# Kernel tuning notes

Hardware: AMD Instinct MI355X
Metric: run time of the kernel (lower is better)

## Reference

```python
import jax, jax.numpy as jnp
import numpy as np

GROUP = 32  # hadamard_group_size == MXFP4 block size
FP4_GRID = np.array([0.0, 0.5, 1.0, 1.5, 2.0, 3.0, 4.0, 6.0], dtype=np.float32)  # e2m1 magnitudes
FP4_MID = np.array([0.25, 0.75, 1.25, 1.75, 2.5, 3.5, 5.0], dtype=np.float32)    # RTN midpoints


def _hadamard(n):
    # Sylvester construction, normalized so H is orthonormal (matches hadamard(n)*n**-0.5)
    H = np.array([[1.0]], dtype=np.float64)
    while H.shape[0] < n:
        H = np.block([[H, H], [H, -H]])
    return (H / np.sqrt(n)).astype(np.float32)


def _pseudo_quant_mxfp4(t, H, gs):
    """Hadamard-rotate per group of 32, then MXFP4 (e2m1 + power-of-two block scale)
    quant-dequant with abs_max scaling and a global scale. STE through the rounding."""
    shp = t.shape
    rot = t.reshape(-1, GROUP) @ H                      # [n_groups, 32] rotated space
    v = jax.lax.stop_gradient(rot) * gs
    absmax = jnp.max(jnp.abs(v), axis=-1, keepdims=True)
    # E8M0 power-of-two shared scale so that absmax/scale <= 6 (max e2m1 value)
    scale = jnp.exp2(jnp.ceil(jnp.log2(absmax / 6.0 + 1e-30)))
    scale = jnp.where(absmax > 0, scale, 1.0)
    u = v / scale
    grid = jnp.asarray(FP4_GRID)
    mid = jnp.asarray(FP4_MID)
    q = jnp.sign(u) * grid[jnp.searchsorted(mid, jnp.abs(u))]  # round-to-nearest e2m1
    dq = q * scale / gs
    out = rot + jax.lax.stop_gradient(dq - rot)         # straight-through estimator
    return out.reshape(shp)


def setup_inputs() -> dict:
    key = jax.random.key(0)
    kx, kw, kb = jax.random.split(key, 3)
    B, S, K, N = 4, 2048, 4096, 4096
    x = jax.random.normal(kx, (B, S, K), jnp.float32)
    weight = jax.random.normal(kw, (N, K), jnp.float32) * (K ** -0.5)
    bias = jax.random.normal(kb, (N,), jnp.float32)
    H = jnp.asarray(_hadamard(GROUP))
    weight_global_scale = jnp.array([3.0], jnp.float32)  # abs_max method
    act_global_scale = jnp.array([3.0], jnp.float32)
    return {"x": x, "weight": weight, "bias": bias, "hadamard_matrix": H,
            "weight_global_scale": weight_global_scale, "act_global_scale": act_global_scale}


def reference(x, weight, bias, hadamard_matrix, weight_global_scale, act_global_scale):
    x_dq = _pseudo_quant_mxfp4(x, hadamard_matrix, act_global_scale[0])
    w_dq = _pseudo_quant_mxfp4(weight, hadamard_matrix, weight_global_scale[0])
    # both operands stay in the rotated space; per-group Hadamard is orthogonal so
    # x_rot @ w_rot^T == x @ w^T up to quantization error (QuTLASS semantics)
    return jnp.einsum('bsk,nk->bsn', x_dq, w_dq) + bias
```

## Files before the change

### kernel.cpp

```cpp
#include <hip/hip_runtime.h>
#include <hip/hip_bf16.h>

typedef int   i32x4  __attribute__((ext_vector_type(4)));
typedef int   i32x8  __attribute__((ext_vector_type(8)));
typedef float f32x16 __attribute__((ext_vector_type(16)));

__device__ inline void gload_lds16(const void* g, void* l) {
  __builtin_amdgcn_global_load_lds((const __attribute__((address_space(1))) void*)g,
                                   (__attribute__((address_space(3))) void*)l, 16, 0, 0);
}
__device__ inline void gload_lds4(const void* g, void* l) {
  __builtin_amdgcn_global_load_lds((const __attribute__((address_space(1))) void*)g,
                                   (__attribute__((address_space(3))) void*)l, 4, 0, 0);
}

__global__ __launch_bounds__(256) void quant_fused(const float* __restrict__ x,
                                                   const float* __restrict__ wt,
                                                   unsigned char* __restrict__ xq,
                                                   unsigned char* __restrict__ xsc,
                                                   unsigned char* __restrict__ wq,
                                                   unsigned char* __restrict__ wsc,
                                                   const float* __restrict__ ags,
                                                   const float* __restrict__ wgs,
                                                   int xg, int Mrows, int Nrows, int kg) {
  const int first = blockIdx.x * 256;
  const bool isX = first < xg;
  const float* in        = isX ? x   : wt;
  unsigned char* outq    = isX ? xq  : wq;
  unsigned char* outsc   = isX ? xsc : wsc;
  const float gs         = isX ? ags[0] : wgs[0];
  const int rows         = isX ? Mrows : Nrows;
  const int base         = isX ? first : first - xg;
  const int g = base + threadIdx.x;
  const int r = g / kg, j = g - r * kg;

  float t[32];
  const float4* p4 = (const float4*)(in + (size_t)g * 32);
#pragma unroll
  for (int i = 0; i < 8; ++i) {
    float4 v4 = p4[i];
    t[4 * i + 0] = v4.x; t[4 * i + 1] = v4.y;
    t[4 * i + 2] = v4.z; t[4 * i + 3] = v4.w;
  }
#pragma unroll
  for (int s = 0; s < 5; ++s) {
    const int hh = 1 << s;
#pragma unroll
    for (int i = 0; i < 32; ++i) {
      if ((i & hh) == 0) {
        float a = t[i], b = t[i + hh];
        t[i] = a + b;
        t[i + hh] = a - b;
      }
    }
  }

  const float c = 0.17677669529663687f;
  float v[32];
  float am = 0.0f;
#pragma unroll
  for (int i = 0; i < 32; ++i) {
    float vi = (t[i] * c) * gs;
    v[i] = vi;
    am = fmaxf(am, fabsf(vi));
  }

  float a6 = am / 6.0f;
  int ex;
  float mant = frexpf(a6, &ex);
  int e = (mant == 0.5f) ? ex - 1 : ex;
  if (e < -127) e = -127;
  if (e > 127) e = 127;
  float inv_s = ldexpf(1.0f, -e);

  unsigned int dw[4] = {0u, 0u, 0u, 0u};
#pragma unroll
  for (int i = 0; i < 32; ++i) {
    float u = v[i] * inv_s;
    float au = fabsf(u);
    int idx = (au > 0.25f) + (au > 0.75f) + (au > 1.25f) + (au > 1.75f)
            + (au > 2.5f) + (au > 3.5f) + (au > 5.0f);
    int code = idx | ((u < 0.0f) ? 8 : 0);
    dw[i >> 3] |= (unsigned)code << ((i & 7) * 4);
  }
  i32x4 packed;
  packed[0] = (int)dw[0]; packed[1] = (int)dw[1];
  packed[2] = (int)dw[2]; packed[3] = (int)dw[3];
  *(i32x4*)(outq + (size_t)r * ((size_t)kg * 16) + (size_t)j * 16) = packed;

  int s = j >> 3, j0 = j & 7;
  int p = ((j0 & 1) << 2) | (j0 >> 1);
  if (kg == 128) {
    __shared__ unsigned char sl[256];
    sl[(s << 4) | ((r & 1) << 3) | p] = (unsigned char)(e + 127);
    __syncthreads();
    if (threadIdx.x < 64) {
      int si = threadIdx.x >> 2, wd = threadIdx.x & 3;
      unsigned int vv = *(const unsigned int*)&sl[(si << 4) | (wd << 2)];
      size_t r0 = (size_t)(base / 128);
      *(unsigned int*)(outsc + ((size_t)si * rows + r0) * 8 + (wd << 2)) = vv;
    }
  } else {
    outsc[((size_t)s * rows + r) * 8 + p] = (unsigned char)(e + 127);
  }
}


#define STAGE(mb, kt, hh, ldsHalf) do {                                              \
    const unsigned char* _s = (mb) + (size_t)((hh)*64 + (w << 3) + (l >> 3)) * KB2   \
                      + (size_t)(kt) * 128 + (size_t)csw * 16;                       \
    gload_lds16(_s, (unsigned char*)(ldsHalf) + (w << 10));                          \
    gload_lds16(_s + ((size_t)KB2 << 5), (unsigned char*)(ldsHalf) + (w << 10) + 4096); \
  } while (0)

#define STAGE_ASC(kt, bf) gload_lds4(AscG + ((size_t)(kt) * M + brow) * 8 + (tid << 2), \
                                     (unsigned char*)&asc[bf][0] + (w << 8))
#define STAGE_BSC(kt, bf) gload_lds4(BscG + ((size_t)(kt) * N + bcol) * 8 + (tid << 2), \
                                     (unsigned char*)&bsc[bf][0] + (w << 8))

#define STAGESET(kt, bf) do {                                                        \
    STAGE(Bb, kt, 0, &lds[bf][1][0]); STAGE(Bb, kt, 1, &lds[bf][1][8192]);           \
    STAGE_BSC(kt, bf);                                                               \
    STAGE(Ab, kt, 0, &lds[bf][0][0]); STAGE(Ab, kt, 1, &lds[bf][0][8192]);           \
    STAGE_ASC(kt, bf);                                                               \
  } while (0)

#define READFRAGS(bf) do {                                                           \
    const unsigned char* _bb = &lds[bf][1][0];                                       \
    _Pragma("unroll")                                                                \
    for (int nt = 0; nt < 2; ++nt) {                                                 \
      int row = wn * 64 + nt * 32 + (l & 31);                                        \
      int xr = row & 7;                                                              \
      _Pragma("unroll")                                                              \
      for (int kk = 0; kk < 4; ++kk)                                                 \
        *(i32x4*)&bf8[nt][kk] = *(const i32x4*)(_bb + row * 128 + (((kk * 2 + h) ^ xr) << 4)); \
      sb[nt] = *(const int*)((const unsigned char*)&bsc[bf][0] + row * 8 + h * 4);   \
    }                                                                                \
    const unsigned char* _ab = &lds[bf][0][0];                                       \
    _Pragma("unroll")                                                                \
    for (int mt = 0; mt < 2; ++mt) {                                                 \
      int row = wm * 64 + mt * 32 + (l & 31);                                        \
      int xr = row & 7;                                                              \
      _Pragma("unroll")                                                              \
      for (int kk = 0; kk < 4; ++kk)                                                 \
        *(i32x4*)&af8[mt][kk] = *(const i32x4*)(_ab + row * 128 + (((kk * 2 + h) ^ xr) << 4)); \
      sa[mt] = *(const int*)((const unsigned char*)&asc[bf][0] + row * 8 + h * 4);   \
    } } while (0)

#define MF1(mt, nt, kk)                                                              \
  acc[mt][nt] = __builtin_amdgcn_mfma_scale_f32_32x32x64_f8f6f4(                     \
      af8[mt][kk], bf8[nt][kk], acc[mt][nt], 4, 4, kk, sa[mt], kk, sb[nt]);

#define MFMAQ16() do {                                                               \
    __builtin_amdgcn_s_setprio(1);                                                   \
    MF1(0, 0, 0) MF1(0, 1, 0) MF1(1, 0, 0) MF1(1, 1, 0)                              \
    MF1(0, 0, 1) MF1(0, 1, 1) MF1(1, 0, 1) MF1(1, 1, 1)                              \
    MF1(0, 0, 2) MF1(0, 1, 2) MF1(1, 0, 2) MF1(1, 1, 2)                              \
    MF1(0, 0, 3) MF1(0, 1, 3) MF1(1, 0, 3) MF1(1, 1, 3)                              \
    __builtin_amdgcn_s_setprio(0);                                                   \
  } while (0)

#define DRAIN_THEN_BAR() do {                                                        \
    asm volatile("s_waitcnt lgkmcnt(0)" ::: "memory");                               \
    __builtin_amdgcn_sched_barrier(0);                                               \
    __builtin_amdgcn_s_barrier();                                                    \
  } while (0)

#define ENDP() __builtin_amdgcn_s_barrier()
#define VM10() asm volatile("s_waitcnt vmcnt(10)" ::: "memory")

__global__ __launch_bounds__(256, 2) void gemm128_fp4(const unsigned char* __restrict__ Aq,
                                                      const unsigned char* __restrict__ Bq,
                                                      const unsigned char* __restrict__ AscG,
                                                      const unsigned char* __restrict__ BscG,
                                                      float* __restrict__ C,
                                                      const float* __restrict__ bias,
                                                      const float* __restrict__ gsx,
                                                      const float* __restrict__ gsw,
                                                      int M, int N, int K) {
  __shared__ __align__(16) unsigned char lds[2][2][16384];
  __shared__ __align__(16) unsigned char asc[2][1024];
  __shared__ __align__(16) unsigned char bsc[2][1024];

  const int tid = threadIdx.x;
  const int w = tid >> 6, l = tid & 63;
  const int wm = w >> 1, wn = w & 1;
  const int h = l >> 5;
  const int csw = (l & 7) ^ (l >> 3);
  const int KB2 = K >> 1;

  const int ntn = N >> 7;
  const int nwg = gridDim.x;
  int r_t, c_t;
  {
    int bid = blockIdx.x;
    if ((nwg & 7) == 0) {
      int x = bid & 7, o = bid >> 3, cpx = nwg >> 3;
      int rpx = cpx / ntn;
      if ((ntn & 7) == 0 && rpx > 0 && (cpx % ntn) == 0) {
        int g8 = o & 7, rr = (o >> 3) % rpx, ss = o / (8 * rpx);
        r_t = x * rpx + rr;
        c_t = ss * 8 + g8;
      } else {
        int lin = x * cpx + o;
        r_t = lin / ntn; c_t = lin % ntn;
      }
    } else {
      r_t = bid / ntn; c_t = bid % ntn;
    }
  }
  const size_t brow = (size_t)r_t * 128;
  const size_t bcol = (size_t)c_t * 128;

  const unsigned char* Ab = Aq + brow * (size_t)KB2;
  const unsigned char* Bb = Bq + bcol * (size_t)KB2;

  f32x16 acc[2][2];
#pragma unroll
  for (int m = 0; m < 2; ++m)
#pragma unroll
    for (int n = 0; n < 2; ++n)
#pragma unroll
      for (int r = 0; r < 16; ++r) acc[m][n][r] = 0.0f;

  i32x8 af8[2][4], bf8[2][4];
#pragma unroll
  for (int mt = 0; mt < 2; ++mt)
#pragma unroll
    for (int kk = 0; kk < 4; ++kk) {
#pragma unroll
      for (int q = 0; q < 8; ++q) { af8[mt][kk][q] = 0; bf8[mt][kk][q] = 0; }
    }
  int sa[2], sb[2];

  const int nkt = K / 256;

  STAGESET(0, 0);
  STAGESET(1, 1);
  VM10();
  __builtin_amdgcn_s_barrier();
  READFRAGS(0);

  for (int t = 0; t < nkt; ++t) {
    const int p = t & 1;
    const int t2 = (t + 2 < nkt) ? t + 2 : nkt - 1;

    DRAIN_THEN_BAR();
    STAGESET(t2, p);
    __builtin_amdgcn_sched_barrier(0);
    MFMAQ16();
    VM10();
    ENDP();
    READFRAGS(p ^ 1);
  }

  const float inv = 1.0f / (gsx[0] * gsw[0]);
#pragma unroll
  for (int nt = 0; nt < 2; ++nt) {
    const int col = (int)bcol + wn * 64 + nt * 32 + (l & 31);
    const float bv = bias[col];
#pragma unroll
    for (int mt = 0; mt < 2; ++mt) {
      const size_t rbase = brow + (size_t)(wm * 64 + mt * 32 + 4 * h);
#pragma unroll
      for (int r = 0; r < 16; ++r) {
        const size_t row = rbase + (r & 3) + 8 * (r >> 2);
        C[row * (size_t)N + col] = acc[mt][nt][r] * inv + bv;
      }
    }
  }
}

extern "C" void kernel_launch(void* const* d_in, const int* in_sizes, int n_in,
                              void* d_out, int out_size, void* d_ws, size_t ws_size,
                              hipStream_t stream) {
  const float* x    = (const float*)d_in[0];
  const float* wgt  = (const float*)d_in[1];
  const float* bias = (const float*)d_in[2];
  const float* wgs  = (const float*)d_in[4];
  const float* ags  = (const float*)d_in[5];

  const int N = in_sizes[2];
  const int K = in_sizes[1] / N;
  const int M = in_sizes[0] / K;
  const int kg = K / 32;

  unsigned char* aq  = (unsigned char*)d_ws;
  unsigned char* bq  = aq + (size_t)M * (K / 2);
  unsigned char* asc = bq + (size_t)N * (K / 2);
  unsigned char* bsc = asc + (size_t)M * kg;

  const int xg = in_sizes[0] / 32;
  const int wg = in_sizes[1] / 32;
  quant_fused<<<dim3((xg + wg) / 256), dim3(256), 0, stream>>>(
      x, wgt, aq, asc, bq, bsc, ags, wgs, xg, M, N, kg);

  dim3 grid((M / 128) * (N / 128));
  gemm128_fp4<<<grid, dim3(256), 0, stream>>>(aq, bq, asc, bsc, (float*)d_out, bias,
                                              ags, wgs, M, N, K);
}
```

Before: 150.6 us.

## Split LDS fragment reads into halves interleaved with MFMA groups

Splits each K-tile's LDS fragment reads into two halves. The second half of the current tile loads while the first half's MFMAs run, and the first half of the next tile loads while the second half's MFMAs run. The loop is unrolled by two with ping-pong scale registers so the next tile's scales do not overwrite the ones still in use. This is meant to hide LDS read latency behind matrix ops, but it adds more waitcnt points and live registers, which could hurt occupancy at 2 blocks per CU.

```diff
diff --git a/kernel.cpp b/kernel.cpp
--- a/kernel.cpp
+++ b/kernel.cpp
@@ -125,16 +125,16 @@
     STAGE_ASC(kt, bf);                                                               \
   } while (0)
 
-#define READFRAGS(bf) do {                                                           \
+#define READFRAGS_H1(bf, SA, SB) do {                                                \
     const unsigned char* _bb = &lds[bf][1][0];                                       \
     _Pragma("unroll")                                                                \
     for (int nt = 0; nt < 2; ++nt) {                                                 \
       int row = wn * 64 + nt * 32 + (l & 31);                                        \
       int xr = row & 7;                                                              \
       _Pragma("unroll")                                                              \
-      for (int kk = 0; kk < 4; ++kk)                                                 \
+      for (int kk = 0; kk < 2; ++kk)                                                 \
         *(i32x4*)&bf8[nt][kk] = *(const i32x4*)(_bb + row * 128 + (((kk * 2 + h) ^ xr) << 4)); \
-      sb[nt] = *(const int*)((const unsigned char*)&bsc[bf][0] + row * 8 + h * 4);   \
+      SB[nt] = *(const int*)((const unsigned char*)&bsc[bf][0] + row * 8 + h * 4);   \
     }                                                                                \
     const unsigned char* _ab = &lds[bf][0][0];                                       \
     _Pragma("unroll")                                                                \
@@ -142,32 +142,70 @@
       int row = wm * 64 + mt * 32 + (l & 31);                                        \
       int xr = row & 7;                                                              \
       _Pragma("unroll")                                                              \
-      for (int kk = 0; kk < 4; ++kk)                                                 \
+      for (int kk = 0; kk < 2; ++kk)                                                 \
         *(i32x4*)&af8[mt][kk] = *(const i32x4*)(_ab + row * 128 + (((kk * 2 + h) ^ xr) << 4)); \
-      sa[mt] = *(const int*)((const unsigned char*)&asc[bf][0] + row * 8 + h * 4);   \
+      SA[mt] = *(const int*)((const unsigned char*)&asc[bf][0] + row * 8 + h * 4);   \
     } } while (0)
 
-#define MF1(mt, nt, kk)                                                              \
+#define READFRAGS_H2(bf) do {                                                        \
+    const unsigned char* _bb = &lds[bf][1][0];                                       \
+    _Pragma("unroll")                                                                \
+    for (int nt = 0; nt < 2; ++nt) {                                                 \
+      int row = wn * 64 + nt * 32 + (l & 31);                                        \
+      int xr = row & 7;                                                              \
+      _Pragma("unroll")                                                              \
+      for (int kk = 2; kk < 4; ++kk)                                                 \
+        *(i32x4*)&bf8[nt][kk] = *(const i32x4*)(_bb + row * 128 + (((kk * 2 + h) ^ xr) << 4)); \
+    }                                                                                \
+    const unsigned char* _ab = &lds[bf][0][0];                                       \
+    _Pragma("unroll")                                                                \
+    for (int mt = 0; mt < 2; ++mt) {                                                 \
+      int row = wm * 64 + mt * 32 + (l & 31);                                        \
+      int xr = row & 7;                                                              \
+      _Pragma("unroll")                                                              \
+      for (int kk = 2; kk < 4; ++kk)                                                 \
+        *(i32x4*)&af8[mt][kk] = *(const i32x4*)(_ab + row * 128 + (((kk * 2 + h) ^ xr) << 4)); \
+    } } while (0)
+
+#define MF1(mt, nt, kk, SA, SB)                                                      \
   acc[mt][nt] = __builtin_amdgcn_mfma_scale_f32_32x32x64_f8f6f4(                     \
-      af8[mt][kk], bf8[nt][kk], acc[mt][nt], 4, 4, kk, sa[mt], kk, sb[nt]);
-
-#define MFMAQ16() do {                                                               \
+      af8[mt][kk], bf8[nt][kk], acc[mt][nt], 4, 4, kk, SA[mt], kk, SB[nt]);
+
+#define MFMAQ_H1(SA, SB) do {                                                        \
     __builtin_amdgcn_s_setprio(1);                                                   \
-    MF1(0, 0, 0) MF1(0, 1, 0) MF1(1, 0, 0) MF1(1, 1, 0)                              \
-    MF1(0, 0, 1) MF1(0, 1, 1) MF1(1, 0, 1) MF1(1, 1, 1)                              \
-    MF1(0, 0, 2) MF1(0, 1, 2) MF1(1, 0, 2) MF1(1, 1, 2)                              \
-    MF1(0, 0, 3) MF1(0, 1, 3) MF1(1, 0, 3) MF1(1, 1, 3)                              \
+    MF1(0, 0, 0, SA, SB) MF1(0, 1, 0, SA, SB) MF1(1, 0, 0, SA, SB) MF1(1, 1, 0, SA, SB) \
+    MF1(0, 0, 1, SA, SB) MF1(0, 1, 1, SA, SB) MF1(1, 0, 1, SA, SB) MF1(1, 1, 1, SA, SB) \
     __builtin_amdgcn_s_setprio(0);                                                   \
   } while (0)
 
-#define DRAIN_THEN_BAR() do {                                                        \
+#define MFMAQ_H2(SA, SB) do {                                                        \
+    __builtin_amdgcn_s_setprio(1);                                                   \
+    MF1(0, 0, 2, SA, SB) MF1(0, 1, 2, SA, SB) MF1(1, 0, 2, SA, SB) MF1(1, 1, 2, SA, SB) \
+    MF1(0, 0, 3, SA, SB) MF1(0, 1, 3, SA, SB) MF1(1, 0, 3, SA, SB) MF1(1, 1, 3, SA, SB) \
+    __builtin_amdgcn_s_setprio(0);                                                   \
+  } while (0)
+
+#define LGKM0() do {                                                                 \
     asm volatile("s_waitcnt lgkmcnt(0)" ::: "memory");                               \
     __builtin_amdgcn_sched_barrier(0);                                               \
-    __builtin_amdgcn_s_barrier();                                                    \
   } while (0)
 
 #define ENDP() __builtin_amdgcn_s_barrier()
 #define VM10() asm volatile("s_waitcnt vmcnt(10)" ::: "memory")
+
+#define TILE(BF, OBF, tstage, CURA, CURB, NXTA, NXTB) do {                           \
+    LGKM0();                                                                         \
+    READFRAGS_H2(BF);                                                                \
+    MFMAQ_H1(CURA, CURB);                                                            \
+    LGKM0();                                                                         \
+    __builtin_amdgcn_s_barrier();                                                    \
+    STAGESET(tstage, BF);                                                            \
+    __builtin_amdgcn_sched_barrier(0);                                               \
+    VM10();                                                                          \
+    ENDP();                                                                          \
+    READFRAGS_H1(OBF, NXTA, NXTB);                                                   \
+    MFMAQ_H2(CURA, CURB);                                                            \
+  } while (0)
 
 __global__ __launch_bounds__(256, 2) void gemm128_fp4(const unsigned char* __restrict__ Aq,
                                                       const unsigned char* __restrict__ Bq,
@@ -231,7 +269,7 @@
 #pragma unroll
       for (int q = 0; q < 8; ++q) { af8[mt][kk][q] = 0; bf8[mt][kk][q] = 0; }
     }
-  int sa[2], sb[2];
+  int saA[2], sbA[2], saB[2], sbB[2];
 
   const int nkt = K / 256;
 
@@ -239,19 +277,15 @@
   STAGESET(1, 1);
   VM10();
   __builtin_amdgcn_s_barrier();
-  READFRAGS(0);
-
-  for (int t = 0; t < nkt; ++t) {
-    const int p = t & 1;
+  READFRAGS_H1(0, saA, sbA);
+
+  for (int s = 0; s < nkt / 2; ++s) {
+    const int t = 2 * s;
     const int t2 = (t + 2 < nkt) ? t + 2 : nkt - 1;
-
-    DRAIN_THEN_BAR();
-    STAGESET(t2, p);
-    __builtin_amdgcn_sched_barrier(0);
-    MFMAQ16();
-    VM10();
-    ENDP();
-    READFRAGS(p ^ 1);
+    const int t3 = (t + 3 < nkt) ? t + 3 : nkt - 1;
+
+    TILE(0, 1, t2, saA, sbA, saB, sbB);
+    TILE(1, 0, t3, saB, sbB, saA, sbA);
   }
 
   const float inv = 1.0f / (gsx[0] * gsw[0]);
```

New measurement: 149.4 us. About the same (-0.8%).
